# Performance work log

Measured on AMD Instinct MI355X. Metric: run time of the kernel, lower is better.

The kernel has to match this reference:

```python
import jax, jax.numpy as jnp
import numpy as np

STATE_DIM = 15


def setup_inputs() -> dict:
    key = jax.random.key(0)
    k1, k2, k3 = jax.random.split(key, 3)
    B, S = 4096, 128
    dba_params = jax.random.normal(k1, (B, S, 32), dtype=jnp.float32)
    imu_measurements = jax.random.normal(k2, (B, S, 6), dtype=jnp.float32)
    gt_state = jax.random.normal(k3, (B, S, STATE_DIM), dtype=jnp.float32)
    return {"dba_params": dba_params, "imu_measurements": imu_measurements, "gt_state": gt_state}


def reference(dba_params, imu_measurements, gt_state):
    # use_gt_init=True path: initial pose (pos + quat) taken from gt_state[:, 0, :7]
    B, S, _ = dba_params.shape
    delta = dba_params[..., :7] * 0.1          # [B, S, 7]
    init_pos = gt_state[:, 0, 0:3]              # [B, 3]
    init_q = gt_state[:, 0, 3:7]                # [B, 4]

    # Positions: pure cumulative sum of deltas (no normalization).
    pos = jnp.concatenate(
        [init_pos[:, None, :],
         init_pos[:, None, :] + jnp.cumsum(delta[:, : S - 1, 0:3], axis=1)],
        axis=1)                                 # [B, S, 3]

    # Quaternions: sequential add + renormalize each step -> lax.scan over S-1.
    def step(q, dq):
        new_q = q + dq
        new_q = new_q / jnp.linalg.norm(new_q, axis=-1, keepdims=True)
        return new_q, new_q

    dq_seq = jnp.swapaxes(delta[:, : S - 1, 3:7], 0, 1)  # [S-1, B, 4]
    _, q_steps = jax.lax.scan(step, init_q, dq_seq)       # [S-1, B, 4]
    quats = jnp.concatenate([init_q[:, None, :], jnp.swapaxes(q_steps, 0, 1)], axis=1)  # [B, S, 4]

    rest = jnp.zeros((B, S, STATE_DIM - 7), dtype=dba_params.dtype)  # channels 7:15 stay zero
    return jnp.concatenate([pos, quats, rest], axis=-1)  # [B, S, 15]
```

## Files before the change

### kernel.cpp

```cpp
#include <hip/hip_runtime.h>

#define SEQ 128
#define SD  15
#define REC 32
#define RPB 4
#define NT  (RPB * SEQ)

__global__ __launch_bounds__(NT, 8) void fused_kernel(const float* __restrict__ dba,
                                                      const float* __restrict__ gt,
                                                      float* __restrict__ out,
                                                      int B) {
    const int tid  = threadIdx.x;
    const int row  = tid >> 7;
    const int s    = tid & (SEQ - 1);
    const int lane = tid & 63;
    const int half = s >> 6;
    const int r    = blockIdx.x * RPB + row;
    const bool valid = (r < B);

    __shared__ float4 sdq  [RPB][SEQ + 1];
    __shared__ float4 squat[RPB][SEQ + 1];
    __shared__ float  ginit[RPB][8];
    __shared__ float  w0tot[RPB][3];

    float d0 = 0.f, d1 = 0.f, d2 = 0.f;
    if (valid) {
        const float* rec = dba + ((size_t)r * SEQ + s) * REC;
        const float4 h0 = *reinterpret_cast<const float4*>(rec);
        const float4 h1 = *reinterpret_cast<const float4*>(rec + 4);
        sdq[row][s] = make_float4(h0.w * 0.1f, h1.x * 0.1f, h1.y * 0.1f, h1.z * 0.1f);
        d0 = h0.x * 0.1f; d1 = h0.y * 0.1f; d2 = h0.z * 0.1f;
        if (s == 0) {
            const float* g = gt + (size_t)r * SEQ * SD;
            *reinterpret_cast<float4*>(&ginit[row][0]) = *reinterpret_cast<const float4*>(g);
            *reinterpret_cast<float4*>(&ginit[row][4]) = *reinterpret_cast<const float4*>(g + 4);
        }
    }

    float ix = d0, iy = d1, iz = d2;
#pragma unroll
    for (int off = 1; off < 64; off <<= 1) {
        const float tx = __shfl_up(ix, off, 64);
        const float ty = __shfl_up(iy, off, 64);
        const float tz = __shfl_up(iz, off, 64);
        if (lane >= off) { ix += tx; iy += ty; iz += tz; }
    }
    if (half == 0 && lane == 63) {
        w0tot[row][0] = ix; w0tot[row][1] = iy; w0tot[row][2] = iz;
    }
    __syncthreads();
    if (half == 1) { ix += w0tot[row][0]; iy += w0tot[row][1]; iz += w0tot[row][2]; }

    if (tid < RPB && blockIdx.x * RPB + tid < B) {
        const float4* srow = sdq[tid];
        float4*       qrow = squat[tid];
        float q0 = ginit[tid][3], q1 = ginit[tid][4],
              q2 = ginit[tid][5], q3 = ginit[tid][6];
        qrow[0] = make_float4(q0, q1, q2, q3);

        float4 ring[8];
#pragma unroll
        for (int u = 0; u < 8; ++u) ring[u] = srow[u];

        for (int w = 0; w < 15; ++w) {
#pragma unroll
            for (int u = 0; u < 8; ++u) {
                const int t = w * 8 + u + 1;
                q0 += ring[u].x; q1 += ring[u].y; q2 += ring[u].z; q3 += ring[u].w;
                ring[u] = srow[w * 8 + u + 8];
                const float a = q0 * q0 + q1 * q1;
                const float b = q2 * q2 + q3 * q3;
                const float inv = __builtin_amdgcn_rsqf(a + b);
                q0 *= inv; q1 *= inv; q2 *= inv; q3 *= inv;
                qrow[t] = make_float4(q0, q1, q2, q3);
            }
        }
#pragma unroll
        for (int u = 0; u < 7; ++u) {
            const int t = 121 + u;
            q0 += ring[u].x; q1 += ring[u].y; q2 += ring[u].z; q3 += ring[u].w;
            const float a = q0 * q0 + q1 * q1;
            const float b = q2 * q2 + q3 * q3;
            const float inv = __builtin_amdgcn_rsqf(a + b);
            q0 *= inv; q1 *= inv; q2 *= inv; q3 *= inv;
            qrow[t] = make_float4(q0, q1, q2, q3);
        }
    }
    __syncthreads();

    if (valid) {
        const float4 q = squat[row][s];
        float* o = out + ((size_t)r * SEQ + s) * SD;
        o[0] = ginit[row][0] + ix - d0;
        o[1] = ginit[row][1] + iy - d1;
        o[2] = ginit[row][2] + iz - d2;
        o[3] = q.x; o[4] = q.y; o[5] = q.z; o[6] = q.w;
#pragma unroll
        for (int k = 7; k < SD; ++k) o[k] = 0.f;
    }
}

extern "C" void kernel_launch(void* const* d_in, const int* in_sizes, int n_in,
                              void* d_out, int out_size, void* d_ws, size_t ws_size,
                              hipStream_t stream) {
    const float* dba = (const float*)d_in[0];
    const float* gt  = (const float*)d_in[2];
    float* out = (float*)d_out;

    const int B = in_sizes[0] / (SEQ * REC);
    const int blocks = (B + RPB - 1) / RPB;
    fused_kernel<<<blocks, NT, 0, stream>>>(dba, gt, out, B);
}
```

Before: 30.33 us.

## Write quaternions directly from scan thread, dropping shared staging and second barrier

The serial quaternion scan now stores each normalized quaternion straight to global output instead of staging it in shared memory, which removes the squat buffer and the second __syncthreads. All other threads write positions and zero channels without waiting for the scan. The prefetch of the next eight deltas is restructured into a double-buffered register batch per window. The cost is that a single thread per row issues strided scalar global stores, which may be poorly coalesced.

```diff
diff --git a/kernel.cpp b/kernel.cpp
--- a/kernel.cpp
+++ b/kernel.cpp
@@ -19,7 +19,6 @@
     const bool valid = (r < B);
 
     __shared__ float4 sdq  [RPB][SEQ + 1];
-    __shared__ float4 squat[RPB][SEQ + 1];
     __shared__ float  ginit[RPB][8];
     __shared__ float  w0tot[RPB][3];
 
@@ -51,52 +50,49 @@
     __syncthreads();
     if (half == 1) { ix += w0tot[row][0]; iy += w0tot[row][1]; iz += w0tot[row][2]; }
 
-    if (tid < RPB && blockIdx.x * RPB + tid < B) {
-        const float4* srow = sdq[tid];
-        float4*       qrow = squat[tid];
-        float q0 = ginit[tid][3], q1 = ginit[tid][4],
-              q2 = ginit[tid][5], q3 = ginit[tid][6];
-        qrow[0] = make_float4(q0, q1, q2, q3);
-
-        float4 ring[8];
-#pragma unroll
-        for (int u = 0; u < 8; ++u) ring[u] = srow[u];
-
-        for (int w = 0; w < 15; ++w) {
-#pragma unroll
-            for (int u = 0; u < 8; ++u) {
-                const int t = w * 8 + u + 1;
-                q0 += ring[u].x; q1 += ring[u].y; q2 += ring[u].z; q3 += ring[u].w;
-                ring[u] = srow[w * 8 + u + 8];
-                const float a = q0 * q0 + q1 * q1;
-                const float b = q2 * q2 + q3 * q3;
-                const float inv = __builtin_amdgcn_rsqf(a + b);
-                q0 *= inv; q1 *= inv; q2 *= inv; q3 *= inv;
-                qrow[t] = make_float4(q0, q1, q2, q3);
-            }
-        }
-#pragma unroll
-        for (int u = 0; u < 7; ++u) {
-            const int t = 121 + u;
-            q0 += ring[u].x; q1 += ring[u].y; q2 += ring[u].z; q3 += ring[u].w;
-            const float a = q0 * q0 + q1 * q1;
-            const float b = q2 * q2 + q3 * q3;
-            const float inv = __builtin_amdgcn_rsqf(a + b);
-            q0 *= inv; q1 *= inv; q2 *= inv; q3 *= inv;
-            qrow[t] = make_float4(q0, q1, q2, q3);
-        }
-    }
-    __syncthreads();
-
     if (valid) {
-        const float4 q = squat[row][s];
         float* o = out + ((size_t)r * SEQ + s) * SD;
         o[0] = ginit[row][0] + ix - d0;
         o[1] = ginit[row][1] + iy - d1;
         o[2] = ginit[row][2] + iz - d2;
-        o[3] = q.x; o[4] = q.y; o[5] = q.z; o[6] = q.w;
+        if (s == 0) {
+            o[3] = ginit[row][3]; o[4] = ginit[row][4];
+            o[5] = ginit[row][5]; o[6] = ginit[row][6];
+        }
 #pragma unroll
         for (int k = 7; k < SD; ++k) o[k] = 0.f;
+    }
+
+    if (tid < RPB && blockIdx.x * RPB + tid < B) {
+        const float4* srow = sdq[tid];
+        float* oq = out + ((size_t)(blockIdx.x * RPB + tid) * SEQ + 1) * SD + 3;
+        float q0 = ginit[tid][3], q1 = ginit[tid][4],
+              q2 = ginit[tid][5], q3 = ginit[tid][6];
+
+#define QSTEP(C) do {                                                   \
+            q0 += (C).x; q1 += (C).y; q2 += (C).z; q3 += (C).w;         \
+            const float a_ = q0 * q0 + q1 * q1;                         \
+            const float b_ = q2 * q2 + q3 * q3;                         \
+            const float i_ = __builtin_amdgcn_rsqf(a_ + b_);            \
+            q0 *= i_; q1 *= i_; q2 *= i_; q3 *= i_;                     \
+            oq[0] = q0; oq[1] = q1; oq[2] = q2; oq[3] = q3;             \
+            oq += SD;                                                   \
+        } while (0)
+
+        float4 c0 = srow[0], c1 = srow[1], c2 = srow[2], c3 = srow[3],
+               c4 = srow[4], c5 = srow[5], c6 = srow[6], c7 = srow[7];
+        for (int w = 0; w < 15; ++w) {
+            const float4* nx = srow + (w + 1) * 8;
+            const float4 n0 = nx[0], n1 = nx[1], n2 = nx[2], n3 = nx[3],
+                         n4 = nx[4], n5 = nx[5], n6 = nx[6], n7 = nx[7];
+            QSTEP(c0); QSTEP(c1); QSTEP(c2); QSTEP(c3);
+            QSTEP(c4); QSTEP(c5); QSTEP(c6); QSTEP(c7);
+            c0 = n0; c1 = n1; c2 = n2; c3 = n3;
+            c4 = n4; c5 = n5; c6 = n6; c7 = n7;
+        }
+        QSTEP(c0); QSTEP(c1); QSTEP(c2); QSTEP(c3);
+        QSTEP(c4); QSTEP(c5); QSTEP(c6);
+#undef QSTEP
     }
 }
 
```

Result: slower. 34.39 us (+13.4%).
